# Kernel tuning notes

Hardware: AMD Instinct MI355X
Metric: run time of the kernel (lower is better)

Reference implementation:

```python
import jax, jax.numpy as jnp
import numpy as np
from jax import lax

DIM = 256
HEADS = 8
WIN = 5
B, H, W = 4, 120, 120


def _templates():
    neg = -0.5
    pos = 1.0 + 1.0 / 3.0
    nor = -3.0 / 8.0
    cnor = 4.0
    nws = [
        [[nor, nor, nor], [nor, cnor, nor], [nor, nor, nor]],
        [[neg, pos, neg], [neg, pos, neg], [neg, pos, neg]],
        [[neg, neg, neg], [pos, pos, pos], [neg, neg, neg]],
        [[pos, neg, neg], [neg, pos, neg], [neg, neg, pos]],
        [[neg, neg, pos], [neg, pos, neg], [pos, neg, neg]],
        [[neg, pos, neg], [pos, pos, neg], [neg, neg, neg]],
        [[neg, pos, neg], [neg, pos, pos], [neg, neg, neg]],
        [[neg, neg, neg], [pos, pos, neg], [neg, pos, neg]],
        [[neg, neg, neg], [neg, pos, pos], [neg, pos, neg]],
    ]
    return np.asarray(nws, dtype=np.float32)  # [9,3,3]


def setup_inputs() -> dict:
    key = jax.random.key(0)
    kx, kk, kv, kq, ko = jax.random.split(key, 5)
    x = jax.random.normal(kx, (B, DIM, H, W), dtype=jnp.float32)
    # depthwise conv templates, tiled per channel: [9, DIM, 1, 3, 3]
    nws = _templates()
    conv_w = jnp.asarray(np.tile(nws[:, None, None, :, :], (1, DIM, 1, 1, 1)))
    s = DIM ** -0.5
    Wk = jax.random.normal(kk, (DIM, DIM), dtype=jnp.float32) * s
    Wv = jax.random.normal(kv, (DIM, DIM), dtype=jnp.float32) * s
    Wq = jax.random.normal(kq, (DIM, DIM), dtype=jnp.float32) * s
    Wout = jax.random.normal(ko, (DIM, DIM), dtype=jnp.float32) * s
    bout = jnp.zeros((DIM,), dtype=jnp.float32)
    return {"x": x, "conv_w": conv_w, "Wk": Wk, "Wv": Wv, "Wq": Wq,
            "Wout": Wout, "bout": bout}


def reference(x, conv_w, Wk, Wv, Wq, Wout, bout):
    b, c, h, w = x.shape
    num = conv_w.shape[0]
    win, heads = WIN, HEADS
    dh = c // heads
    scale = dh ** -0.5
    b1, b2 = h // win, w // win

    # 9 depthwise 3x3 convs (padding=1), concatenated on channel dim
    kvs = [lax.conv_general_dilated(x, conv_w[i], (1, 1), "SAME",
                                    feature_group_count=c)
           for i in range(num)]
    pm = jnp.concatenate(kvs, axis=1)  # [b, num*c, h, w]

    kv0 = pm.reshape(b, num, c, b1, win, b2, win)
    kv0 = kv0.transpose(0, 3, 5, 1, 4, 6, 2).reshape(b * b1 * b2, num * win * win, c)
    q0 = x.reshape(b, c, b1, win, b2, win)
    q0 = q0.transpose(0, 2, 4, 3, 5, 1).reshape(b * b1 * b2, win * win, c)

    def heads_split(t):  # [B_, n, c] -> [B_, heads, n, dh]
        return t.reshape(t.shape[0], t.shape[1], heads, dh).transpose(0, 2, 1, 3)

    kh = heads_split(kv0 @ Wk.T)
    vh = heads_split(kv0 @ Wv.T)
    qh = heads_split(q0 @ Wq.T) * scale

    attn = jax.nn.softmax(jnp.einsum("bhqd,bhkd->bhqk", qh, kh), axis=-1)
    out = jnp.einsum("bhqk,bhkd->bhqd", attn, vh)          # [B_, heads, 25, dh]
    out = out.transpose(0, 2, 1, 3).reshape(b * b1 * b2, win * win, c)
    out = out @ Wout.T + bout

    # window merge back to NCHW
    out = out.reshape(b, b1, b2, win, win, c)
    out = out.transpose(0, 5, 1, 3, 2, 4).reshape(b, c, h, w)
    return out
```

## Files before the change

kernel.cpp:

```cpp
#include <hip/hip_runtime.h>

#define IMGW 120
#define IMGH 120
#define NPIX 14400
#define XS   460800

typedef unsigned short u16;
typedef short bf16x8 __attribute__((ext_vector_type(8)));
typedef float f32x4 __attribute__((ext_vector_type(4)));

__device__ inline u16 f2bf(float f) {
  unsigned int x = __float_as_uint(f);
  unsigned int r = x + 0x7FFFu + ((x >> 16) & 1u);
  return (u16)(r >> 16);
}
__device__ inline unsigned int pk2(float a, float b) {
  return (unsigned int)f2bf(a) | ((unsigned int)f2bf(b) << 16);
}
__device__ inline float bf2f(u16 h) { return __uint_as_float(((unsigned int)h) << 16); }

__global__ __launch_bounds__(256) void wconv_kernel(
    const float* __restrict__ Wq, const float* __restrict__ Wk,
    const float* __restrict__ Wv, const float* __restrict__ Wo,
    u16* __restrict__ Wb)
{
  const int t = threadIdx.x, bx = blockIdx.x, mat = blockIdx.y;
  const float* src = mat == 0 ? Wq : mat == 1 ? Wk : mat == 2 ? Wv : Wo;
  const float sc = (mat == 0) ? 0.17677669529663687f : 1.0f;
  const int e0 = (bx * 256 + t) * 4;
  float4 v = *(const float4*)(src + e0);
  uint2 u;
  u.x = pk2(v.x * sc, v.y * sc);
  u.y = pk2(v.z * sc, v.w * sc);
  *(uint2*)(Wb + (size_t)mat * 65536 + e0) = u;
}

__global__ __launch_bounds__(256) void xpose_kernel(
    const float* __restrict__ x, u16* __restrict__ x_t)
{
  __shared__ u16 sh[64 * 66];
  const int t = threadIdx.x;
  const int p0 = blockIdx.x * 64;
  const int b  = blockIdx.y;
  const int c0 = blockIdx.z * 64;
  const float* xb = x + ((size_t)b * 256 + c0) * NPIX + p0;
  #pragma unroll
  for (int it = 0; it < 16; ++it) {
    int ch = it * 4 + (t >> 6), pix = t & 63;
    sh[pix * 66 + ch] = f2bf(xb[(size_t)ch * NPIX + pix]);
  }
  __syncthreads();
  u16* ob = x_t + ((size_t)b * NPIX + p0) * 256 + c0;
  const unsigned int* sh32 = (const unsigned int*)sh;
  #pragma unroll
  for (int it = 0; it < 8; ++it) {
    int flat = it * 256 + t;
    int pix = flat >> 5, c2 = flat & 31;
    ((unsigned int*)(ob + (size_t)pix * 256))[c2] = sh32[pix * 33 + c2];
  }
}

__global__ __launch_bounds__(256) void projmm_kernel(
    const u16* __restrict__ x_t, const u16* __restrict__ Wb,
    u16* __restrict__ Qb, u16* __restrict__ Kb, u16* __restrict__ Vb)
{
  __shared__ u16 Ws[256 * 40];
  __shared__ u16 Xs[64 * 40];
  const int t = threadIdx.x;
  const int lane = t & 63, wv = t >> 6;
  const int p0 = blockIdx.x * 64;
  const int b  = blockIdx.y;
  const int mat = blockIdx.z;

  const u16* Wm = Wb + (size_t)mat * 65536;
  const u16* Xb = x_t + ((size_t)b * NPIX + p0) * 256;

  f32x4 acc[4][4];
  #pragma unroll
  for (int i = 0; i < 4; ++i)
    #pragma unroll
    for (int j = 0; j < 4; ++j) acc[i][j] = {0.f, 0.f, 0.f, 0.f};

  for (int kk = 0; kk < 8; ++kk) {
    #pragma unroll
    for (int p = 0; p < 4; ++p) {
      int fl = t + 256 * p;
      int d = fl >> 2, c = fl & 3;
      uint4 u = *(const uint4*)(Wm + d * 256 + kk * 32 + c * 8);
      *(uint4*)&Ws[d * 40 + c * 8] = u;
    }
    {
      int pix = t >> 2, c = t & 3;
      uint4 u = *(const uint4*)(Xb + (size_t)pix * 256 + kk * 32 + c * 8);
      *(uint4*)&Xs[pix * 40 + c * 8] = u;
    }
    __syncthreads();
    bf16x8 af[4], bfr[4];
    #pragma unroll
    for (int f = 0; f < 4; ++f)
      af[f] = *(const bf16x8*)&Ws[(wv * 64 + f * 16 + (lane & 15)) * 40 + (lane >> 4) * 8];
    #pragma unroll
    for (int f = 0; f < 4; ++f)
      bfr[f] = *(const bf16x8*)&Xs[(f * 16 + (lane & 15)) * 40 + (lane >> 4) * 8];
    #pragma unroll
    for (int df = 0; df < 4; ++df)
      #pragma unroll
      for (int pf = 0; pf < 4; ++pf)
        acc[df][pf] = __builtin_amdgcn_mfma_f32_16x16x32_bf16(af[df], bfr[pf], acc[df][pf], 0, 0, 0);
    __syncthreads();
  }

  u16* O = (mat == 0) ? Qb : (mat == 1) ? Kb : Vb;
  #pragma unroll
  for (int df = 0; df < 4; ++df) {
    int dim0 = wv * 64 + df * 16 + (lane >> 4) * 4;
    int h = dim0 >> 5, dl0 = dim0 & 31;
    #pragma unroll
    for (int pf = 0; pf < 4; ++pf) {
      int pix = p0 + pf * 16 + (lane & 15);
      f32x4 v = acc[df][pf];
      uint2 u;
      u.x = pk2(v[0], v[1]);
      u.y = pk2(v[2], v[3]);
      *(uint2*)&O[((size_t)(b * 8 + h) * NPIX + pix) * 32 + dl0] = u;
    }
  }
}

__global__ __launch_bounds__(64, 3) void attn_kernel(
    const u16* __restrict__ Qb,
    const u16* __restrict__ Kb,
    const u16* __restrict__ Vb,
    u16* __restrict__ AO)
{
  __shared__ __align__(16) unsigned char smem[11536];
  float* SA   = (float*)smem;
  u16*   vsT  = (u16*)(smem + 6800);
  float* drow = (float*)(smem + 11408);

  const int lane = threadIdx.x;
  const int bid = blockIdx.x;
  const int h = bid / 2304;
  const int w = bid % 2304;
  const int b = w / 576;
  const int rr = w % 576;
  const int by = rr / 24, bx = rr % 24;
  const int y0 = by * 5, x0 = bx * 5;
  const size_t gbase = (size_t)(b * 8 + h) * XS;
  const u16* Qg = Qb + gbase;
  const u16* Kg = Kb + gbase;
  const u16* Vg = Vb + gbase;

  const int cc = lane & 15, kgrp = lane >> 4;
  const int ks8 = kgrp * 8;
  const int r0 = kgrp * 4;
  const int kpl = lane & 31;

  if (lane >= 25 && lane < 32) drow[lane] = 0.f;

  bf16x8 aq0, aq1;
  {
    int rA = cc;
    int wyA = (rA * 13) >> 6, wxA = rA - wyA * 5;
    uint4 uA = *(const uint4*)(Qg + (size_t)((y0 + wyA) * IMGW + x0 + wxA) * 32 + ks8);
    aq0 = *(bf16x8*)&uA;
    int rB = cc + 16; int rBc = rB < 25 ? rB : 0;
    int wyB = (rBc * 13) >> 6, wxB = rBc - wyB * 5;
    uint4 uB = *(const uint4*)(Qg + (size_t)((y0 + wyB) * IMGW + x0 + wxB) * 32 + ks8);
    aq1 = *(bf16x8*)&uB;
  }

  bf16x8 bk[4];
  #pragma unroll
  for (int nt = 0; nt < 4; ++nt) {
    int pp = cc + nt * 16;
    int hy = (pp * 37) >> 8, hx = pp - hy * 7;
    int gy = y0 - 1 + hy, gx = x0 - 1 + hx;
    bool inb = (gy >= 0) && (gy < IMGH) && (gx >= 0) && (gx < IMGW);
    int gyc = min(max(gy, 0), IMGH - 1), gxc = min(max(gx, 0), IMGW - 1);
    uint4 u = *(const uint4*)(Kg + (size_t)(gyc * IMGW + gxc) * 32 + ks8);
    if (pp < 49 && !inb) u = make_uint4(0u, 0u, 0u, 0u);
    bk[nt] = *(bf16x8*)&u;
  }

  #pragma unroll
  for (int it = 0; it < 4; ++it) {
    int f = lane + 64 * it;
    int pp = f >> 2, c = f & 3;
    int hy = (pp * 37) >> 8, hx = pp - hy * 7;
    int gy = y0 - 1 + hy, gx = x0 - 1 + hx;
    uint4 u = make_uint4(0u, 0u, 0u, 0u);
    if (pp < 49 && gy >= 0 && gy < IMGH && gx >= 0 && gx < IMGW)
      u = *(const uint4*)(Vg + (size_t)(gy * IMGW + gx) * 32 + c * 8);
    const int d0 = c * 8;
    vsT[(d0 + 0) * 72 + pp] = (u16)(u.x & 0xffff);
    vsT[(d0 + 1) * 72 + pp] = (u16)(u.x >> 16);
    vsT[(d0 + 2) * 72 + pp] = (u16)(u.y & 0xffff);
    vsT[(d0 + 3) * 72 + pp] = (u16)(u.y >> 16);
    vsT[(d0 + 4) * 72 + pp] = (u16)(u.z & 0xffff);
    vsT[(d0 + 5) * 72 + pp] = (u16)(u.z >> 16);
    vsT[(d0 + 6) * 72 + pp] = (u16)(u.w & 0xffff);
    vsT[(d0 + 7) * 72 + pp] = (u16)(u.w >> 16);
  }

  {
    const f32x4 z = {0.f, 0.f, 0.f, 0.f};
    f32x4 s[2][4];
    #pragma unroll
    for (int nt = 0; nt < 4; ++nt) {
      s[0][nt] = __builtin_amdgcn_mfma_f32_16x16x32_bf16(aq0, bk[nt], z, 0, 0, 0);
      s[1][nt] = __builtin_amdgcn_mfma_f32_16x16x32_bf16(aq1, bk[nt], z, 0, 0, 0);
    }
    #pragma unroll
    for (int mt = 0; mt < 2; ++mt)
      #pragma unroll
      for (int nt = 0; nt < 4; ++nt)
        #pragma unroll
        for (int i = 0; i < 4; ++i) {
          int q = mt * 16 + r0 + i, pp = nt * 16 + cc;
          if (q < 25 && pp < 49) SA[q * 68 + pp] = s[mt][nt][i];
        }
  }

  int idxA[9], idxB[9];
  float selA[9], selB[9];
  {
    const int hb = lane & 32;
    const int ppA = kpl, ppB = 32 + kpl;
    const int hyA = (ppA * 37) >> 8, hxA = ppA - hyA * 7;
    const int hyB = (ppB * 37) >> 8, hxB = ppB - hyB * 7;
    #pragma unroll
    for (int dy = 0; dy < 3; ++dy)
      #pragma unroll
      for (int dx = 0; dx < 3; ++dx) {
        int j = dy * 3 + dx;
        int kyA = hyA - dy, kxA = hxA - dx;
        bool vA = ((unsigned)kyA < 5u) && ((unsigned)kxA < 5u);
        idxA[j] = (hb + (vA ? kyA * 5 + kxA : 0)) << 2;
        selA[j] = vA ? 1.f : 0.f;
        int kyB = hyB - dy, kxB = hxB - dx;
        bool vB = ((unsigned)kyB < 5u) && ((unsigned)kxB < 5u);
        idxB[j] = (hb + (vB ? kyB * 5 + kxB : 0)) << 2;
        selB[j] = vB ? 1.f : 0.f;
      }
  }

  const float DPN = 11.f / 6.f;
  const float LOG2E = 1.44269504f;
  const int kyq = (kpl * 13) >> 6, kxq = kpl - kyq * 5;
  const int sboff = kyq * 7 + kxq;

  for (int t = 0; t < 13; ++t) {
    const int q = 2 * t + (lane >> 5);
    const bool act = (kpl < 25) && (q < 25);
    const float* sp = SA + q * 68 + sboff;
    float s0 = sp[0], s1 = sp[1], s2 = sp[2];
    float s3 = sp[7], s4 = sp[8], s5 = sp[9];
    float s6 = sp[14], s7 = sp[15], s8 = sp[16];

    float st = ((s0 + s1) + (s2 + s3)) + ((s5 + s6) + (s7 + s8)) + s4;
    float l0 = -0.375f * st + 4.375f * s4;
    float base = -0.5f * st + DPN * s4;
    float l1 = base + DPN * (s1 + s7);
    float l2 = base + DPN * (s3 + s5);
    float l3 = base + DPN * (s0 + s8);
    float l4 = base + DPN * (s2 + s6);
    float l5 = base + DPN * (s1 + s3);
    float l6 = base + DPN * (s1 + s5);
    float l7 = base + DPN * (s3 + s7);
    float l8 = base + DPN * (s5 + s7);

    float p0 = exp2f(fmaf(l0, LOG2E, -32.f));
    float p1 = exp2f(fmaf(l1, LOG2E, -32.f));
    float p2 = exp2f(fmaf(l2, LOG2E, -32.f));
    float p3 = exp2f(fmaf(l3, LOG2E, -32.f));
    float p4 = exp2f(fmaf(l4, LOG2E, -32.f));
    float p5 = exp2f(fmaf(l5, LOG2E, -32.f));
    float p6 = exp2f(fmaf(l6, LOG2E, -32.f));
    float p7 = exp2f(fmaf(l7, LOG2E, -32.f));
    float p8 = exp2f(fmaf(l8, LOG2E, -32.f));
    float ps = ((p0 + p1) + (p2 + p3)) + ((p4 + p5) + (p6 + p7)) + p8;

    float sv = act ? ps : 0.f;
    sv += __int_as_float(__builtin_amdgcn_update_dpp(0, __float_as_int(sv), 0xB1, 0xF, 0xF, true));
    sv += __int_as_float(__builtin_amdgcn_update_dpp(0, __float_as_int(sv), 0x4E, 0xF, 0xF, true));
    sv += __shfl_xor(sv, 4);
    sv += __shfl_xor(sv, 8);
    sv += __shfl_xor(sv, 16);
    if (kpl == 0 && q < 25) drow[q] = __builtin_amdgcn_rcpf(sv + 1e-35f);

    float psm0 = ps - p0;
    float basec = -0.5f * psm0 - 0.375f * p0;
    float cv[9];
    cv[0] = basec + DPN * p3;
    cv[1] = basec + DPN * ((p1 + p5) + p6);
    cv[2] = basec + DPN * p4;
    cv[3] = basec + DPN * ((p2 + p5) + p7);
    cv[4] = 4.f * p0 + (4.f / 3.f) * psm0;
    cv[5] = basec + DPN * ((p2 + p6) + p8);
    cv[6] = basec + DPN * p4;
    cv[7] = basec + DPN * ((p1 + p7) + p8);
    cv[8] = basec + DPN * p3;

    float a = 0.f, a2 = 0.f;
    #pragma unroll
    for (int j = 0; j < 9; ++j) {
      int cj = __float_as_int(cv[j]);
      a  = fmaf(selA[j], __int_as_float(__builtin_amdgcn_ds_bpermute(idxA[j], cj)), a);
      a2 = fmaf(selB[j], __int_as_float(__builtin_amdgcn_ds_bpermute(idxB[j], cj)), a2);
    }

    if (q < 25) {
      u16* arow = (u16*)((char*)SA + q * 272);
      u16 h1 = f2bf(a);
      arow[kpl]      = h1;
      arow[64 + kpl] = f2bf(a - bf2f(h1));
      u16 h2 = f2bf(a2);
      arow[32 + kpl] = h2;
      arow[96 + kpl] = f2bf(a2 - bf2f(h2));
    }
  }

  __syncthreads();

  {
    f32x4 o[2][2];
    #pragma unroll
    for (int i = 0; i < 2; ++i)
      #pragma unroll
      for (int j = 0; j < 2; ++j) o[i][j] = {0.f, 0.f, 0.f, 0.f};
    #pragma unroll
    for (int kx = 0; kx < 2; ++kx) {
      const int koff = kx * 64 + kgrp * 16;
      const char* sa = (const char*)SA;
      bf16x8 ah0 = *(const bf16x8*)(sa + cc * 272 + koff);
      bf16x8 ah1 = *(const bf16x8*)(sa + (cc + 16) * 272 + koff);
      bf16x8 al0 = *(const bf16x8*)(sa + cc * 272 + 128 + koff);
      bf16x8 al1 = *(const bf16x8*)(sa + (cc + 16) * 272 + 128 + koff);
      bf16x8 b0  = *(const bf16x8*)&vsT[cc * 72 + kx * 32 + ks8];
      bf16x8 b1  = *(const bf16x8*)&vsT[(cc + 16) * 72 + kx * 32 + ks8];
      o[0][0] = __builtin_amdgcn_mfma_f32_16x16x32_bf16(ah0, b0, o[0][0], 0, 0, 0);
      o[0][0] = __builtin_amdgcn_mfma_f32_16x16x32_bf16(al0, b0, o[0][0], 0, 0, 0);
      o[0][1] = __builtin_amdgcn_mfma_f32_16x16x32_bf16(ah0, b1, o[0][1], 0, 0, 0);
      o[0][1] = __builtin_amdgcn_mfma_f32_16x16x32_bf16(al0, b1, o[0][1], 0, 0, 0);
      o[1][0] = __builtin_amdgcn_mfma_f32_16x16x32_bf16(ah1, b0, o[1][0], 0, 0, 0);
      o[1][0] = __builtin_amdgcn_mfma_f32_16x16x32_bf16(al1, b0, o[1][0], 0, 0, 0);
      o[1][1] = __builtin_amdgcn_mfma_f32_16x16x32_bf16(ah1, b1, o[1][1], 0, 0, 0);
      o[1][1] = __builtin_amdgcn_mfma_f32_16x16x32_bf16(al1, b1, o[1][1], 0, 0, 0);
    }
    #pragma unroll
    for (int mt = 0; mt < 2; ++mt) {
      float4 rv = *(const float4*)&drow[mt * 16 + r0];
      #pragma unroll
      for (int i = 0; i < 4; ++i) {
        int q = mt * 16 + r0 + i;
        if (q < 25) {
          int qy = (q * 13) >> 6, qx = q - qy * 5;
          u16* dst = AO + gbase + ((size_t)((y0 + qy) * IMGW + x0 + qx)) * 32;
          float r = (&rv.x)[i];
          dst[cc]      = f2bf(o[mt][0][i] * r);
          dst[cc + 16] = f2bf(o[mt][1][i] * r);
        }
      }
    }
  }
}

__global__ __launch_bounds__(256) void outmm_kernel(
    const u16* __restrict__ AOb, const u16* __restrict__ Wb,
    const float* __restrict__ bout, float* __restrict__ O)
{
  __shared__ u16 Ws[256 * 40];
  __shared__ u16 Xs[64 * 40];
  const int t = threadIdx.x;
  const int lane = t & 63, wv = t >> 6;
  const int p0 = blockIdx.x * 64;
  const int b  = blockIdx.y;
  const u16* Wm = Wb + (size_t)3 * 65536;

  f32x4 acc[4][4];
  #pragma unroll
  for (int i = 0; i < 4; ++i)
    #pragma unroll
    for (int j = 0; j < 4; ++j) acc[i][j] = {0.f, 0.f, 0.f, 0.f};

  for (int kk = 0; kk < 8; ++kk) {
    #pragma unroll
    for (int p = 0; p < 4; ++p) {
      int fl = t + 256 * p;
      int d = fl >> 2, c = fl & 3;
      uint4 u = *(const uint4*)(Wm + d * 256 + kk * 32 + c * 8);
      *(uint4*)&Ws[d * 40 + c * 8] = u;
    }
    {
      int pix = t >> 2, c = t & 3;
      uint4 u = *(const uint4*)(AOb + ((size_t)(b * 8 + kk) * NPIX + p0 + pix) * 32 + c * 8);
      *(uint4*)&Xs[pix * 40 + c * 8] = u;
    }
    __syncthreads();
    bf16x8 af[4], bfr[4];
    #pragma unroll
    for (int f = 0; f < 4; ++f)
      af[f] = *(const bf16x8*)&Ws[(wv * 64 + f * 16 + (lane & 15)) * 40 + (lane >> 4) * 8];
    #pragma unroll
    for (int f = 0; f < 4; ++f)
      bfr[f] = *(const bf16x8*)&Xs[(f * 16 + (lane & 15)) * 40 + (lane >> 4) * 8];
    #pragma unroll
    for (int df = 0; df < 4; ++df)
      #pragma unroll
      for (int pf = 0; pf < 4; ++pf)
        acc[df][pf] = __builtin_amdgcn_mfma_f32_16x16x32_bf16(af[df], bfr[pf], acc[df][pf], 0, 0, 0);
    __syncthreads();
  }

  #pragma unroll
  for (int df = 0; df < 4; ++df) {
    int dim0 = wv * 64 + df * 16 + (lane >> 4) * 4;
    float4 bv = *(const float4*)&bout[dim0];
    #pragma unroll
    for (int pf = 0; pf < 4; ++pf) {
      int pix = p0 + pf * 16 + (lane & 15);
      f32x4 v = acc[df][pf];
      float* ob = O + (size_t)b * 256 * NPIX + pix;
      ob[(size_t)(dim0 + 0) * NPIX] = v[0] + bv.x;
      ob[(size_t)(dim0 + 1) * NPIX] = v[1] + bv.y;
      ob[(size_t)(dim0 + 2) * NPIX] = v[2] + bv.z;
      ob[(size_t)(dim0 + 3) * NPIX] = v[3] + bv.w;
    }
  }
}

extern "C" void kernel_launch(void* const* d_in, const int* in_sizes, int n_in,
                              void* d_out, int out_size, void* d_ws, size_t ws_size,
                              hipStream_t stream) {
  const float* x    = (const float*)d_in[0];
  const float* Wk   = (const float*)d_in[2];
  const float* Wv   = (const float*)d_in[3];
  const float* Wq   = (const float*)d_in[4];
  const float* Wout = (const float*)d_in[5];
  const float* bout = (const float*)d_in[6];

  u16* x_t = (u16*)d_out;
  u16* Qb  = x_t + (size_t)4 * NPIX * 256;
  u16* Kb  = (u16*)d_ws;
  u16* Vb  = Kb + (size_t)4 * NPIX * 256;
  u16* AOb = Vb + (size_t)4 * NPIX * 256;
  u16* Wb  = AOb + (size_t)4 * NPIX * 256;

  wconv_kernel<<<dim3(64, 4), 256, 0, stream>>>(Wq, Wk, Wv, Wout, Wb);
  xpose_kernel<<<dim3(225, 4, 4), 256, 0, stream>>>(x, x_t);
  projmm_kernel<<<dim3(225, 4, 3), 256, 0, stream>>>(x_t, Wb, Qb, Kb, Vb);
  attn_kernel<<<dim3(18432), 64, 0, stream>>>(Qb, Kb, Vb, AOb);
  outmm_kernel<<<dim3(225, 4), 256, 0, stream>>>(AOb, Wb, bout, (float*)d_out);
}
```

Before: 219.7 us.

## Fuse transpose into projection GEMM and load weights directly from global

The separate transpose/bf16 conversion kernel is removed. The projection kernel now reads fp32 x directly, converts and transposes one 64-pixel tile of all 256 channels into shared memory once, and reuses it for Q, K and V in a loop over the three weight matrices. Both GEMM kernels now load weight and activation fragments straight from global memory into registers instead of staging through shared memory with barriers. This removes a kernel launch, the x_t round trip and the sync overhead. In exchange it gives up grid parallelism (a third as many projection blocks) and relies on L2/L1 caching for repeated weight reads.

```diff
diff --git a/kernel.cpp b/kernel.cpp
--- a/kernel.cpp
+++ b/kernel.cpp
@@ -35,94 +35,71 @@
   *(uint2*)(Wb + (size_t)mat * 65536 + e0) = u;
 }
 
-__global__ __launch_bounds__(256) void xpose_kernel(
-    const float* __restrict__ x, u16* __restrict__ x_t)
+__global__ __launch_bounds__(256) void projmm_kernel(
+    const float* __restrict__ x, const u16* __restrict__ Wb,
+    u16* __restrict__ Qb, u16* __restrict__ Kb, u16* __restrict__ Vb)
 {
-  __shared__ u16 sh[64 * 66];
+  __shared__ u16 Xf[64 * 264];
   const int t = threadIdx.x;
+  const int lane = t & 63, wv = t >> 6;
+  const int cc = lane & 15, kgrp = lane >> 4;
   const int p0 = blockIdx.x * 64;
   const int b  = blockIdx.y;
-  const int c0 = blockIdx.z * 64;
-  const float* xb = x + ((size_t)b * 256 + c0) * NPIX + p0;
-  #pragma unroll
-  for (int it = 0; it < 16; ++it) {
-    int ch = it * 4 + (t >> 6), pix = t & 63;
-    sh[pix * 66 + ch] = f2bf(xb[(size_t)ch * NPIX + pix]);
+  const float* xb = x + (size_t)b * 256 * NPIX + p0;
+
+  {
+    unsigned int* X32 = (unsigned int*)Xf;
+    const int pix4 = t & 15;
+    #pragma unroll
+    for (int it = 0; it < 8; ++it) {
+      int j = (t >> 4) + it * 16;
+      float4 va = *(const float4*)(xb + (size_t)(2 * j) * NPIX + pix4 * 4);
+      float4 vb = *(const float4*)(xb + (size_t)(2 * j + 1) * NPIX + pix4 * 4);
+      X32[(pix4 * 4 + 0) * 132 + j] = pk2(va.x, vb.x);
+      X32[(pix4 * 4 + 1) * 132 + j] = pk2(va.y, vb.y);
+      X32[(pix4 * 4 + 2) * 132 + j] = pk2(va.z, vb.z);
+      X32[(pix4 * 4 + 3) * 132 + j] = pk2(va.w, vb.w);
+    }
   }
   __syncthreads();
-  u16* ob = x_t + ((size_t)b * NPIX + p0) * 256 + c0;
-  const unsigned int* sh32 = (const unsigned int*)sh;
-  #pragma unroll
-  for (int it = 0; it < 8; ++it) {
-    int flat = it * 256 + t;
-    int pix = flat >> 5, c2 = flat & 31;
-    ((unsigned int*)(ob + (size_t)pix * 256))[c2] = sh32[pix * 33 + c2];
-  }
-}
-
-__global__ __launch_bounds__(256) void projmm_kernel(
-    const u16* __restrict__ x_t, const u16* __restrict__ Wb,
-    u16* __restrict__ Qb, u16* __restrict__ Kb, u16* __restrict__ Vb)
-{
-  __shared__ u16 Ws[256 * 40];
-  __shared__ u16 Xs[64 * 40];
-  const int t = threadIdx.x;
-  const int lane = t & 63, wv = t >> 6;
-  const int p0 = blockIdx.x * 64;
-  const int b  = blockIdx.y;
-  const int mat = blockIdx.z;
-
-  const u16* Wm = Wb + (size_t)mat * 65536;
-  const u16* Xb = x_t + ((size_t)b * NPIX + p0) * 256;
-
-  f32x4 acc[4][4];
-  #pragma unroll
-  for (int i = 0; i < 4; ++i)
-    #pragma unroll
-    for (int j = 0; j < 4; ++j) acc[i][j] = {0.f, 0.f, 0.f, 0.f};
-
-  for (int kk = 0; kk < 8; ++kk) {
-    #pragma unroll
-    for (int p = 0; p < 4; ++p) {
-      int fl = t + 256 * p;
-      int d = fl >> 2, c = fl & 3;
-      uint4 u = *(const uint4*)(Wm + d * 256 + kk * 32 + c * 8);
-      *(uint4*)&Ws[d * 40 + c * 8] = u;
-    }
-    {
-      int pix = t >> 2, c = t & 3;
-      uint4 u = *(const uint4*)(Xb + (size_t)pix * 256 + kk * 32 + c * 8);
-      *(uint4*)&Xs[pix * 40 + c * 8] = u;
-    }
-    __syncthreads();
-    bf16x8 af[4], bfr[4];
-    #pragma unroll
-    for (int f = 0; f < 4; ++f)
-      af[f] = *(const bf16x8*)&Ws[(wv * 64 + f * 16 + (lane & 15)) * 40 + (lane >> 4) * 8];
-    #pragma unroll
-    for (int f = 0; f < 4; ++f)
-      bfr[f] = *(const bf16x8*)&Xs[(f * 16 + (lane & 15)) * 40 + (lane >> 4) * 8];
-    #pragma unroll
-    for (int df = 0; df < 4; ++df)
-      #pragma unroll
-      for (int pf = 0; pf < 4; ++pf)
-        acc[df][pf] = __builtin_amdgcn_mfma_f32_16x16x32_bf16(af[df], bfr[pf], acc[df][pf], 0, 0, 0);
-    __syncthreads();
-  }
-
-  u16* O = (mat == 0) ? Qb : (mat == 1) ? Kb : Vb;
-  #pragma unroll
-  for (int df = 0; df < 4; ++df) {
-    int dim0 = wv * 64 + df * 16 + (lane >> 4) * 4;
-    int h = dim0 >> 5, dl0 = dim0 & 31;
-    #pragma unroll
-    for (int pf = 0; pf < 4; ++pf) {
-      int pix = p0 + pf * 16 + (lane & 15);
-      f32x4 v = acc[df][pf];
-      uint2 u;
-      u.x = pk2(v[0], v[1]);
-      u.y = pk2(v[2], v[3]);
-      *(uint2*)&O[((size_t)(b * 8 + h) * NPIX + pix) * 32 + dl0] = u;
+
+  for (int mat = 0; mat < 3; ++mat) {
+    const u16* Wm = Wb + (size_t)mat * 65536;
+    f32x4 acc[4][4];
+    #pragma unroll
+    for (int i = 0; i < 4; ++i)
+      #pragma unroll
+      for (int j = 0; j < 4; ++j) acc[i][j] = {0.f, 0.f, 0.f, 0.f};
+
+    for (int kk = 0; kk < 8; ++kk) {
+      bf16x8 af[4], bfr[4];
+      #pragma unroll
+      for (int f = 0; f < 4; ++f)
+        af[f] = *(const bf16x8*)(Wm + (size_t)(wv * 64 + f * 16 + cc) * 256 + kk * 32 + kgrp * 8);
+      #pragma unroll
+      for (int nt = 0; nt < 4; ++nt)
+        bfr[nt] = *(const bf16x8*)&Xf[(nt * 16 + cc) * 264 + kk * 32 + kgrp * 8];
+      #pragma unroll
+      for (int df = 0; df < 4; ++df)
+        #pragma unroll
+        for (int pf = 0; pf < 4; ++pf)
+          acc[df][pf] = __builtin_amdgcn_mfma_f32_16x16x32_bf16(af[df], bfr[pf], acc[df][pf], 0, 0, 0);
+    }
+
+    u16* O = (mat == 0) ? Qb : (mat == 1) ? Kb : Vb;
+    #pragma unroll
+    for (int df = 0; df < 4; ++df) {
+      int dim0 = wv * 64 + df * 16 + kgrp * 4;
+      int h = dim0 >> 5, dl0 = dim0 & 31;
+      #pragma unroll
+      for (int pf = 0; pf < 4; ++pf) {
+        int pix = p0 + pf * 16 + cc;
+        f32x4 v = acc[df][pf];
+        uint2 u;
+        u.x = pk2(v[0], v[1]);
+        u.y = pk2(v[2], v[3]);
+        *(uint2*)&O[((size_t)(b * 8 + h) * NPIX + pix) * 32 + dl0] = u;
+      }
     }
   }
 }
@@ -370,10 +347,9 @@
     const u16* __restrict__ AOb, const u16* __restrict__ Wb,
     const float* __restrict__ bout, float* __restrict__ O)
 {
-  __shared__ u16 Ws[256 * 40];
-  __shared__ u16 Xs[64 * 40];
   const int t = threadIdx.x;
   const int lane = t & 63, wv = t >> 6;
+  const int cc = lane & 15, kgrp = lane >> 4;
   const int p0 = blockIdx.x * 64;
   const int b  = blockIdx.y;
   const u16* Wm = Wb + (size_t)3 * 65536;
@@ -385,41 +361,27 @@
     for (int j = 0; j < 4; ++j) acc[i][j] = {0.f, 0.f, 0.f, 0.f};
 
   for (int kk = 0; kk < 8; ++kk) {
-    #pragma unroll
-    for (int p = 0; p < 4; ++p) {
-      int fl = t + 256 * p;
-      int d = fl >> 2, c = fl & 3;
-      uint4 u = *(const uint4*)(Wm + d * 256 + kk * 32 + c * 8);
-      *(uint4*)&Ws[d * 40 + c * 8] = u;
-    }
-    {
-      int pix = t >> 2, c = t & 3;
-      uint4 u = *(const uint4*)(AOb + ((size_t)(b * 8 + kk) * NPIX + p0 + pix) * 32 + c * 8);
-      *(uint4*)&Xs[pix * 40 + c * 8] = u;
-    }
-    __syncthreads();
     bf16x8 af[4], bfr[4];
     #pragma unroll
     for (int f = 0; f < 4; ++f)
-      af[f] = *(const bf16x8*)&Ws[(wv * 64 + f * 16 + (lane & 15)) * 40 + (lane >> 4) * 8];
-    #pragma unroll
-    for (int f = 0; f < 4; ++f)
-      bfr[f] = *(const bf16x8*)&Xs[(f * 16 + (lane & 15)) * 40 + (lane >> 4) * 8];
+      af[f] = *(const bf16x8*)(Wm + (size_t)(wv * 64 + f * 16 + cc) * 256 + kk * 32 + kgrp * 8);
+    #pragma unroll
+    for (int nt = 0; nt < 4; ++nt)
+      bfr[nt] = *(const bf16x8*)(AOb + ((size_t)(b * 8 + kk) * NPIX + p0 + nt * 16 + cc) * 32 + kgrp * 8);
     #pragma unroll
     for (int df = 0; df < 4; ++df)
       #pragma unroll
       for (int pf = 0; pf < 4; ++pf)
         acc[df][pf] = __builtin_amdgcn_mfma_f32_16x16x32_bf16(af[df], bfr[pf], acc[df][pf], 0, 0, 0);
-    __syncthreads();
   }
 
   #pragma unroll
   for (int df = 0; df < 4; ++df) {
-    int dim0 = wv * 64 + df * 16 + (lane >> 4) * 4;
+    int dim0 = wv * 64 + df * 16 + kgrp * 4;
     float4 bv = *(const float4*)&bout[dim0];
     #pragma unroll
     for (int pf = 0; pf < 4; ++pf) {
-      int pix = p0 + pf * 16 + (lane & 15);
+      int pix = p0 + pf * 16 + cc;
       f32x4 v = acc[df][pf];
       float* ob = O + (size_t)b * 256 * NPIX + pix;
       ob[(size_t)(dim0 + 0) * NPIX] = v[0] + bv.x;
@@ -440,16 +402,14 @@
   const float* Wout = (const float*)d_in[5];
   const float* bout = (const float*)d_in[6];
 
-  u16* x_t = (u16*)d_out;
-  u16* Qb  = x_t + (size_t)4 * NPIX * 256;
+  u16* Qb  = (u16*)d_out;
   u16* Kb  = (u16*)d_ws;
   u16* Vb  = Kb + (size_t)4 * NPIX * 256;
   u16* AOb = Vb + (size_t)4 * NPIX * 256;
   u16* Wb  = AOb + (size_t)4 * NPIX * 256;
 
   wconv_kernel<<<dim3(64, 4), 256, 0, stream>>>(Wq, Wk, Wv, Wout, Wb);
-  xpose_kernel<<<dim3(225, 4, 4), 256, 0, stream>>>(x, x_t);
-  projmm_kernel<<<dim3(225, 4, 3), 256, 0, stream>>>(x_t, Wb, Qb, Kb, Vb);
+  projmm_kernel<<<dim3(225, 4), 256, 0, stream>>>(x, Wb, Qb, Kb, Vb);
   attn_kernel<<<dim3(18432), 64, 0, stream>>>(Qb, Kb, Vb, AOb);
   outmm_kernel<<<dim3(225, 4), 256, 0, stream>>>(AOb, Wb, bout, (float*)d_out);
 }
```

Measured after the change: 210.1 us. 1.05x faster.
